# Optimization experiments

Measured on AMD Instinct MI355X. Metric: run time of the kernel, lower is better.

The kernel has to match this reference:

```python
import jax, jax.numpy as jnp
import numpy as np

DIM = 1024
HEADS = 16
HEAD_DIM = DIM // HEADS
SCALE = HEAD_DIM ** -0.5


def setup_inputs() -> dict:
    key = jax.random.key(0)
    ks = jax.random.split(key, 6)
    B, N = 2, 2048
    s = DIM ** -0.5
    return {
        "x": jax.random.normal(ks[0], (B, N, DIM), dtype=jnp.float32),
        "Wq": jax.random.normal(ks[1], (DIM, DIM), dtype=jnp.float32) * s,
        "Wk": jax.random.normal(ks[2], (DIM, DIM), dtype=jnp.float32) * s,
        "Wv": jax.random.normal(ks[3], (DIM, DIM), dtype=jnp.float32) * s,
        "Wo": jax.random.normal(ks[4], (DIM, DIM), dtype=jnp.float32) * s,
        "bo": jnp.zeros((DIM,), dtype=jnp.float32),
    }


def reference(x, Wq, Wk, Wv, Wo, bo):
    B, N, D = x.shape
    # Linear projections (torch Linear: y = x @ W.T)
    q = x @ Wq.T
    k = x @ Wk.T
    v = x @ Wv.T
    # [B, H, N, hd]
    q = q.reshape(B, N, HEADS, HEAD_DIM).transpose(0, 2, 1, 3)
    k = k.reshape(B, N, HEADS, HEAD_DIM).transpose(0, 2, 1, 3)
    v = v.reshape(B, N, HEADS, HEAD_DIM).transpose(0, 2, 1, 3)
    scores = jnp.einsum('bhid,bhjd->bhij', q, k) * SCALE
    probs = jax.nn.softmax(scores, axis=-1)
    out = jnp.einsum('bhij,bhjd->bhid', probs, v)
    out = out.transpose(0, 2, 1, 3).reshape(B, N, D)
    return out @ Wo.T + bo
```

## Files before the change

kernel.cpp:

```cpp
#include <hip/hip_runtime.h>

#define DIM    1024
#define HEADS  16
#define HD     64
#define BATCH  2
#define SEQ    2048
#define C2     0.18033688011112042f

typedef __attribute__((ext_vector_type(8))) short           short8;
typedef __attribute__((ext_vector_type(4))) short           short4v;
typedef __attribute__((ext_vector_type(4))) float           f4;
typedef __attribute__((ext_vector_type(4))) unsigned short  u16x4;
typedef __attribute__((ext_vector_type(4))) unsigned int    u32x4;
typedef __attribute__((ext_vector_type(2))) unsigned int    u32x2;

typedef __attribute__((address_space(3))) unsigned int       as3_u32;
typedef const __attribute__((address_space(1))) unsigned int as1_u32;

__device__ __forceinline__ unsigned short f2bf(float f) {
    unsigned int u = __builtin_bit_cast(unsigned int, f);
    u = (u + 0x7fffu + ((u >> 16) & 1u)) >> 16;
    return (unsigned short)u;
}
__device__ __forceinline__ unsigned int pk_bf16(float a, float b) {
    return (unsigned int)f2bf(a) | ((unsigned int)f2bf(b) << 16);
}
__device__ __forceinline__ unsigned int pk_bf16_hw(float a, float b) {
    unsigned int r;
    asm("v_cvt_pk_bf16_f32 %0, %1, %2" : "=v"(r) : "v"(a), "v"(b));
    return r;
}

#if __has_builtin(__builtin_amdgcn_exp2f)
#define EXP2(x) __builtin_amdgcn_exp2f(x)
#else
#define EXP2(x) exp2f(x)
#endif

__device__ __forceinline__ void gl2lds16(const unsigned short* g, unsigned short* l) {
    __builtin_amdgcn_global_load_lds((as1_u32*)g, (as3_u32*)l, 16, 0, 0);
}

__global__ __launch_bounds__(256) void k_cast_all(
    const float* __restrict__ x,  const float* __restrict__ wq,
    const float* __restrict__ wk, const float* __restrict__ wv,
    const float* __restrict__ wo, unsigned short* __restrict__ dst)
{
    const int i = blockIdx.x * 256 + threadIdx.x;
    const float* src;
    int off;
    if (i < (1 << 20))            { src = x;  off = 0; }
    else if (i < (5 << 18))       { src = wq; off = 1 << 20; }
    else if (i < (6 << 18))       { src = wk; off = 5 << 18; }
    else if (i < (7 << 18))       { src = wv; off = 6 << 18; }
    else                          { src = wo; off = 7 << 18; }
    f4 v = ((const f4*)src)[i - off];
    u16x4 o;
    o[0] = f2bf(v[0]); o[1] = f2bf(v[1]); o[2] = f2bf(v[2]); o[3] = f2bf(v[3]);
    ((u16x4*)dst)[i] = o;
}

__global__ __launch_bounds__(256) void gemm_qkv(
    const unsigned short* __restrict__ A,
    const unsigned short* __restrict__ Wq,
    const unsigned short* __restrict__ Wk,
    const unsigned short* __restrict__ Wv,
    unsigned short* __restrict__ Qo,
    unsigned short* __restrict__ Ko,
    unsigned short* __restrict__ Vo)
{
    __shared__ __align__(16) unsigned short Xs[128 * 32];
    __shared__ __align__(16) unsigned short Ws[128 * 32];
    const int L   = blockIdx.x;
    const int xcd = L & 7;
    const int idx = L >> 3;
    const int col = idx >> 2;
    const int sb  = (xcd * 4 + (idx & 3)) * 128;
    const int wsel = col >> 3;
    const int fb   = (col & 7) * 128;
    const unsigned short* W = (wsel == 0) ? Wq : ((wsel == 1) ? Wk : Wv);

    const int tid  = threadIdx.x;
    const int wave = tid >> 6, lane = tid & 63;
    const int quad = lane >> 4, l16 = lane & 15;
    const int wm = (wave & 1) << 6, wn = (wave >> 1) << 6;

    const unsigned short* aLDS = (wsel < 2) ? Ws : Xs;
    const unsigned short* bLDS = (wsel < 2) ? Xs : Ws;

    f4 acc[4][4] = {};

    for (int k0 = 0; k0 < DIM; k0 += 32) {
        __syncthreads();
        #pragma unroll
        for (int i = 0; i < 2; i++) {
            const int c = tid + (i << 8);
            const int row = c >> 2, koff = (c & 3) << 3;
            gl2lds16(&A[(size_t)(sb + row) * DIM + k0 + koff], &Xs[(size_t)((i << 8) + (wave << 6)) * 8]);
            gl2lds16(&W[(size_t)(fb + row) * DIM + k0 + koff], &Ws[(size_t)((i << 8) + (wave << 6)) * 8]);
        }
        __syncthreads();
        short8 afr[4], bfr[4];
        #pragma unroll
        for (int i = 0; i < 4; i++)
            afr[i] = *(const short8*)(&aLDS[(wm + i * 16 + l16) * 32 + quad * 8]);
        #pragma unroll
        for (int j = 0; j < 4; j++)
            bfr[j] = *(const short8*)(&bLDS[(wn + j * 16 + l16) * 32 + quad * 8]);
        #pragma unroll
        for (int i = 0; i < 4; i++)
            #pragma unroll
            for (int j = 0; j < 4; j++)
                acc[i][j] = __builtin_amdgcn_mfma_f32_16x16x32_bf16(afr[i], bfr[j], acc[i][j], 0, 0, 0);
    }

    if (wsel < 2) {
        unsigned short* out = (wsel == 0) ? Qo : Ko;
        const float sc = (wsel == 0) ? C2 : 1.0f;
        #pragma unroll
        for (int j = 0; j < 4; j++) {
            const int ms = sb + wn + j * 16 + l16;
            const int b = ms >> 11, ns = ms & (SEQ - 1);
            #pragma unroll
            for (int i = 0; i < 4; i++) {
                const int feat = fb + wm + i * 16 + quad * 4;
                const int h = feat >> 6, d = feat & (HD - 1);
                u32x2 pw;
                pw[0] = pk_bf16(acc[i][j][0] * sc, acc[i][j][1] * sc);
                pw[1] = pk_bf16(acc[i][j][2] * sc, acc[i][j][3] * sc);
                *(u32x2*)(&out[((size_t)(b * HEADS + h) * SEQ + ns) * HD + d]) = pw;
            }
        }
    } else {
        #pragma unroll
        for (int j = 0; j < 4; j++) {
            const int feat = fb + wn + j * 16 + l16;
            const int h = feat >> 6, d = feat & (HD - 1);
            #pragma unroll
            for (int i = 0; i < 4; i++) {
                const int ms = sb + wm + i * 16 + quad * 4;
                const int b = ms >> 11, ns = ms & (SEQ - 1);
                u32x2 pw;
                pw[0] = pk_bf16(acc[i][j][0], acc[i][j][1]);
                pw[1] = pk_bf16(acc[i][j][2], acc[i][j][3]);
                *(u32x2*)(&Vo[((size_t)(b * HEADS + h) * HD + d) * SEQ + ns]) = pw;
            }
        }
    }
}

__global__ __launch_bounds__(256, 2) void attn_fwd(
    const unsigned short* __restrict__ Qg,
    const unsigned short* __restrict__ Kg,
    const unsigned short* __restrict__ VTg,
    unsigned short* __restrict__ AOb)
{
    __shared__ __align__(16) unsigned short Ks [2][64 * 72];
    __shared__ __align__(16) unsigned short VsT[2][64 * 72];
#if !__has_builtin(__builtin_amdgcn_mfma_f32_16x16x16bf16_1k)
    __shared__ __align__(16) unsigned short Ps[128 * 72];
#endif

    const int L   = blockIdx.x;
    const int xcd = L & 7;
    const int idx = L >> 3;
    const int bh  = xcd * 4 + (idx >> 4);
    const int q0  = (idx & 15) << 7;

    const unsigned short* Qb  = Qg  + (size_t)bh * SEQ * HD;
    const unsigned short* Kb  = Kg  + (size_t)bh * SEQ * HD;
    const unsigned short* VTb = VTg + (size_t)bh * HD * SEQ;

    const int tid  = threadIdx.x;
    const int wave = tid >> 6, lane = tid & 63;
    const int quad = lane >> 4, l16 = lane & 15;
    const int qw   = wave << 5;
    const int r8   = tid >> 3;
    const int g8   = (tid & 7) * 8;

    short8 qf[2][2];
    #pragma unroll
    for (int nf = 0; nf < 2; nf++)
        #pragma unroll
        for (int ks = 0; ks < 2; ks++)
            qf[nf][ks] = *(const short8*)(&Qb[(size_t)(q0 + qw + nf * 16 + l16) * HD + ks * 32 + quad * 8]);

    #pragma unroll
    for (int p = 0; p < 2; p++) {
        const int row = r8 + p * 32;
        *(u32x4*)(&Ks [0][row * 72 + g8]) = *(const u32x4*)(&Kb [(size_t)row * HD + g8]);
        *(u32x4*)(&VsT[0][row * 72 + g8]) = *(const u32x4*)(&VTb[(size_t)row * SEQ + g8]);
    }
    __syncthreads();

    f4 lsum[2] = {};
    f4 Oacc[4][2] = {};
    int cur = 0;

    for (int kt = 0; kt < SEQ / 64; kt++) {
        u32x4 kpre[2], vpre[2];
        if (kt < SEQ / 64 - 1) {
            #pragma unroll
            for (int p = 0; p < 2; p++) {
                const int row = r8 + p * 32;
                kpre[p] = *(const u32x4*)(&Kb [(size_t)((kt + 1) * 64 + row) * HD + g8]);
                vpre[p] = *(const u32x4*)(&VTb[(size_t)row * SEQ + (kt + 1) * 64 + g8]);
            }
        }
        const unsigned short* ksb = &Ks [cur][0];
        const unsigned short* vsb = &VsT[cur][0];

        f4 sacc[4][2] = {};
        __builtin_amdgcn_s_setprio(1);
        #pragma unroll
        for (int ks = 0; ks < 2; ks++) {
            short8 kfr[4];
            #pragma unroll
            for (int mf = 0; mf < 4; mf++)
                kfr[mf] = *(const short8*)(&ksb[(mf * 16 + l16) * 72 + ks * 32 + quad * 8]);
            #pragma unroll
            for (int mf = 0; mf < 4; mf++)
                #pragma unroll
                for (int nf = 0; nf < 2; nf++)
                    sacc[mf][nf] = __builtin_amdgcn_mfma_f32_16x16x32_bf16(kfr[mf], qf[nf][ks], sacc[mf][nf], 0, 0, 0);
        }
        __builtin_amdgcn_s_setprio(0);

#if __has_builtin(__builtin_amdgcn_mfma_f32_16x16x16bf16_1k)
        #pragma unroll
        for (int mf = 0; mf < 4; mf++) {
            short4v vfr[4];
            #pragma unroll
            for (int d = 0; d < 4; d++)
                vfr[d] = *(const short4v*)(&vsb[(d * 16 + l16) * 72 + mf * 16 + quad * 4]);
            short4v pbx[2];
            #pragma unroll
            for (int nf = 0; nf < 2; nf++) {
                f4 pv;
                #pragma unroll
                for (int r = 0; r < 4; r++)
                    pv[r] = EXP2(sacc[mf][nf][r]);
                lsum[nf] += pv;
                u32x2 pw;
                pw[0] = pk_bf16_hw(pv[0], pv[1]);
                pw[1] = pk_bf16_hw(pv[2], pv[3]);
                pbx[nf] = __builtin_bit_cast(short4v, pw);
            }
            #pragma unroll
            for (int d = 0; d < 4; d++)
                #pragma unroll
                for (int nf = 0; nf < 2; nf++)
                    Oacc[d][nf] = __builtin_amdgcn_mfma_f32_16x16x16bf16_1k(vfr[d], pbx[nf], Oacc[d][nf], 0, 0, 0);
        }
#else
        #pragma unroll
        for (int nf = 0; nf < 2; nf++) {
            #pragma unroll
            for (int mf = 0; mf < 4; mf++) {
                f4 pv;
                #pragma unroll
                for (int r = 0; r < 4; r++)
                    pv[r] = EXP2(sacc[mf][nf][r]);
                lsum[nf] += pv;
                u32x2 pw;
                pw[0] = pk_bf16(pv[0], pv[1]);
                pw[1] = pk_bf16(pv[2], pv[3]);
                *(u32x2*)(&Ps[(qw + nf * 16 + l16) * 72 + mf * 16 + quad * 4]) = pw;
            }
        }
        #pragma unroll
        for (int ks = 0; ks < 2; ks++) {
            short8 vfr[4], pf[2];
            #pragma unroll
            for (int mf = 0; mf < 4; mf++)
                vfr[mf] = *(const short8*)(&vsb[(mf * 16 + l16) * 72 + ks * 32 + quad * 8]);
            #pragma unroll
            for (int nf = 0; nf < 2; nf++)
                pf[nf] = *(const short8*)(&Ps[(qw + nf * 16 + l16) * 72 + ks * 32 + quad * 8]);
            #pragma unroll
            for (int mf = 0; mf < 4; mf++)
                #pragma unroll
                for (int nf = 0; nf < 2; nf++)
                    Oacc[mf][nf] = __builtin_amdgcn_mfma_f32_16x16x32_bf16(vfr[mf], pf[nf], Oacc[mf][nf], 0, 0, 0);
        }
#endif

        if (kt < SEQ / 64 - 1) {
            #pragma unroll
            for (int p = 0; p < 2; p++) {
                const int row = r8 + p * 32;
                *(u32x4*)(&Ks [cur ^ 1][row * 72 + g8]) = kpre[p];
                *(u32x4*)(&VsT[cur ^ 1][row * 72 + g8]) = vpre[p];
            }
            __syncthreads();
        }
        cur ^= 1;
    }

    const int b = bh >> 4, h = bh & (HEADS - 1);
    #pragma unroll
    for (int nf = 0; nf < 2; nf++) {
        float l = lsum[nf][0] + lsum[nf][1] + lsum[nf][2] + lsum[nf][3];
        l += __shfl_xor(l, 16);
        l += __shfl_xor(l, 32);
        const float inv = 1.0f / l;
        const int qg = q0 + qw + nf * 16 + l16;
        #pragma unroll
        for (int mf = 0; mf < 4; mf++) {
            u32x2 o;
            o[0] = pk_bf16_hw(Oacc[mf][nf][0] * inv, Oacc[mf][nf][1] * inv);
            o[1] = pk_bf16_hw(Oacc[mf][nf][2] * inv, Oacc[mf][nf][3] * inv);
            *(u32x2*)(&AOb[(size_t)(b * SEQ + qg) * DIM + h * HD + mf * 16 + quad * 4]) = o;
        }
    }
}

__global__ __launch_bounds__(256) void gemm_out(
    const unsigned short* __restrict__ AO,
    const unsigned short* __restrict__ W,
    float* __restrict__ out,
    const float* __restrict__ bias)
{
    __shared__ __align__(16) unsigned short As[64 * 32];
    __shared__ __align__(16) unsigned short Bs[128 * 32];
    const int L   = blockIdx.x;
    const int xcd = L & 7;
    const int idx = L >> 3;
    const int n0  = (xcd * 4 + (idx >> 4)) * 128;
    const int m0  = (idx & 15) * 64;

    const int tid  = threadIdx.x;
    const int wave = tid >> 6, lane = tid & 63;
    const int quad = lane >> 4, l16 = lane & 15;
    const int wm = (wave & 1) << 5, wn = (wave >> 1) << 6;

    f4 acc[2][4] = {};

    for (int k0 = 0; k0 < DIM; k0 += 32) {
        __syncthreads();
        gl2lds16(&W[(size_t)(m0 + (tid >> 2)) * DIM + k0 + ((tid & 3) << 3)],
                 &As[(size_t)(wave << 6) * 8]);
        #pragma unroll
        for (int i = 0; i < 2; i++) {
            const int c = tid + (i << 8);
            gl2lds16(&AO[(size_t)(n0 + (c >> 2)) * DIM + k0 + ((c & 3) << 3)],
                     &Bs[(size_t)((i << 8) + (wave << 6)) * 8]);
        }
        __syncthreads();
        short8 afr[2], bfr[4];
        #pragma unroll
        for (int i = 0; i < 2; i++)
            afr[i] = *(const short8*)(&As[(wm + i * 16 + l16) * 32 + quad * 8]);
        #pragma unroll
        for (int j = 0; j < 4; j++)
            bfr[j] = *(const short8*)(&Bs[(wn + j * 16 + l16) * 32 + quad * 8]);
        #pragma unroll
        for (int i = 0; i < 2; i++)
            #pragma unroll
            for (int j = 0; j < 4; j++)
                acc[i][j] = __builtin_amdgcn_mfma_f32_16x16x32_bf16(afr[i], bfr[j], acc[i][j], 0, 0, 0);
    }

    #pragma unroll
    for (int i = 0; i < 2; i++) {
        const int feat = m0 + wm + i * 16 + quad * 4;
        const f4 bv = *(const f4*)(&bias[feat]);
        #pragma unroll
        for (int j = 0; j < 4; j++) {
            const int ns = n0 + wn + j * 16 + l16;
            *(f4*)(&out[(size_t)ns * DIM + feat]) = acc[i][j] + bv;
        }
    }
}

extern "C" void kernel_launch(void* const* d_in, const int* in_sizes, int n_in,
                              void* d_out, int out_size, void* d_ws, size_t ws_size,
                              hipStream_t stream) {
    (void)in_sizes; (void)n_in; (void)out_size; (void)ws_size;
    const float* x  = (const float*)d_in[0];
    const float* Wq = (const float*)d_in[1];
    const float* Wk = (const float*)d_in[2];
    const float* Wv = (const float*)d_in[3];
    const float* Wo = (const float*)d_in[4];
    const float* bo = (const float*)d_in[5];

    unsigned short* wsu = (unsigned short*)d_ws;
    unsigned short* xb  = wsu;
    unsigned short* Wqb = wsu + (4u  << 20);
    unsigned short* Wkb = wsu + (5u  << 20);
    unsigned short* Wvb = wsu + (6u  << 20);
    unsigned short* Wob = wsu + (7u  << 20);
    unsigned short* Qb  = wsu + (8u  << 20);
    unsigned short* Kb  = wsu + (12u << 20);
    unsigned short* VTb = wsu + (16u << 20);
    unsigned short* AOb = wsu + (20u << 20);

    k_cast_all<<<8192, 256, 0, stream>>>(x, Wq, Wk, Wv, Wo, wsu);

    gemm_qkv<<<768, 256, 0, stream>>>(xb, Wqb, Wkb, Wvb, Qb, Kb, VTb);

    attn_fwd<<<512, 256, 0, stream>>>(Qb, Kb, VTb, AOb);

    gemm_out<<<512, 256, 0, stream>>>(AOb, Wob, (float*)d_out, bo);
}
```

Measured before the change: 179.7 us.

## Double-buffer LDS tiles in QKV and output projection GEMMs

Both projection GEMMs now keep two LDS tile buffers. The global-to-LDS load for the next k-step is issued before the MFMAs on the current buffer, and the loop drops from two barriers per iteration to one. The aim is to hide global load latency behind matrix math. LDS use per block doubles, which may lower occupancy, and correctness depends on the barrier also waiting for the async LDS-DMA loads to finish.

Result: slower. 183.6 us (+2.2%).

```diff
diff --git a/kernel.cpp b/kernel.cpp
--- a/kernel.cpp
+++ b/kernel.cpp
@@ -69,8 +69,8 @@
     unsigned short* __restrict__ Ko,
     unsigned short* __restrict__ Vo)
 {
-    __shared__ __align__(16) unsigned short Xs[128 * 32];
-    __shared__ __align__(16) unsigned short Ws[128 * 32];
+    __shared__ __align__(16) unsigned short Xs[2][128 * 32];
+    __shared__ __align__(16) unsigned short Ws[2][128 * 32];
     const int L   = blockIdx.x;
     const int xcd = L & 7;
     const int idx = L >> 3;
@@ -85,21 +85,27 @@
     const int quad = lane >> 4, l16 = lane & 15;
     const int wm = (wave & 1) << 6, wn = (wave >> 1) << 6;
 
-    const unsigned short* aLDS = (wsel < 2) ? Ws : Xs;
-    const unsigned short* bLDS = (wsel < 2) ? Xs : Ws;
-
-    f4 acc[4][4] = {};
-
-    for (int k0 = 0; k0 < DIM; k0 += 32) {
-        __syncthreads();
+    auto STAGE = [&](int buf, int k0) {
         #pragma unroll
         for (int i = 0; i < 2; i++) {
             const int c = tid + (i << 8);
             const int row = c >> 2, koff = (c & 3) << 3;
-            gl2lds16(&A[(size_t)(sb + row) * DIM + k0 + koff], &Xs[(size_t)((i << 8) + (wave << 6)) * 8]);
-            gl2lds16(&W[(size_t)(fb + row) * DIM + k0 + koff], &Ws[(size_t)((i << 8) + (wave << 6)) * 8]);
-        }
-        __syncthreads();
+            gl2lds16(&A[(size_t)(sb + row) * DIM + k0 + koff], &Xs[buf][(size_t)((i << 8) + (wave << 6)) * 8]);
+            gl2lds16(&W[(size_t)(fb + row) * DIM + k0 + koff], &Ws[buf][(size_t)((i << 8) + (wave << 6)) * 8]);
+        }
+    };
+
+    f4 acc[4][4] = {};
+    int cur = 0;
+
+    STAGE(0, 0);
+    asm volatile("s_waitcnt vmcnt(0)" ::: "memory");
+    __syncthreads();
+
+    for (int k0 = 0; k0 < DIM; k0 += 32) {
+        if (k0 + 32 < DIM) STAGE(cur ^ 1, k0 + 32);
+        const unsigned short* aLDS = (wsel < 2) ? &Ws[cur][0] : &Xs[cur][0];
+        const unsigned short* bLDS = (wsel < 2) ? &Xs[cur][0] : &Ws[cur][0];
         short8 afr[4], bfr[4];
         #pragma unroll
         for (int i = 0; i < 4; i++)
@@ -112,6 +118,8 @@
             #pragma unroll
             for (int j = 0; j < 4; j++)
                 acc[i][j] = __builtin_amdgcn_mfma_f32_16x16x32_bf16(afr[i], bfr[j], acc[i][j], 0, 0, 0);
+        __syncthreads();
+        cur ^= 1;
     }
 
     if (wsel < 2) {
@@ -321,8 +329,8 @@
     float* __restrict__ out,
     const float* __restrict__ bias)
 {
-    __shared__ __align__(16) unsigned short As[64 * 32];
-    __shared__ __align__(16) unsigned short Bs[128 * 32];
+    __shared__ __align__(16) unsigned short As[2][64 * 32];
+    __shared__ __align__(16) unsigned short Bs[2][128 * 32];
     const int L   = blockIdx.x;
     const int xcd = L & 7;
     const int idx = L >> 3;
@@ -334,31 +342,40 @@
     const int quad = lane >> 4, l16 = lane & 15;
     const int wm = (wave & 1) << 5, wn = (wave >> 1) << 6;
 
-    f4 acc[2][4] = {};
-
-    for (int k0 = 0; k0 < DIM; k0 += 32) {
-        __syncthreads();
+    auto STAGE = [&](int buf, int k0) {
         gl2lds16(&W[(size_t)(m0 + (tid >> 2)) * DIM + k0 + ((tid & 3) << 3)],
-                 &As[(size_t)(wave << 6) * 8]);
+                 &As[buf][(size_t)(wave << 6) * 8]);
         #pragma unroll
         for (int i = 0; i < 2; i++) {
             const int c = tid + (i << 8);
             gl2lds16(&AO[(size_t)(n0 + (c >> 2)) * DIM + k0 + ((c & 3) << 3)],
-                     &Bs[(size_t)((i << 8) + (wave << 6)) * 8]);
-        }
-        __syncthreads();
+                     &Bs[buf][(size_t)((i << 8) + (wave << 6)) * 8]);
+        }
+    };
+
+    f4 acc[2][4] = {};
+    int cur = 0;
+
+    STAGE(0, 0);
+    asm volatile("s_waitcnt vmcnt(0)" ::: "memory");
+    __syncthreads();
+
+    for (int k0 = 0; k0 < DIM; k0 += 32) {
+        if (k0 + 32 < DIM) STAGE(cur ^ 1, k0 + 32);
         short8 afr[2], bfr[4];
         #pragma unroll
         for (int i = 0; i < 2; i++)
-            afr[i] = *(const short8*)(&As[(wm + i * 16 + l16) * 32 + quad * 8]);
+            afr[i] = *(const short8*)(&As[cur][(wm + i * 16 + l16) * 32 + quad * 8]);
         #pragma unroll
         for (int j = 0; j < 4; j++)
-            bfr[j] = *(const short8*)(&Bs[(wn + j * 16 + l16) * 32 + quad * 8]);
+            bfr[j] = *(const short8*)(&Bs[cur][(wn + j * 16 + l16) * 32 + quad * 8]);
         #pragma unroll
         for (int i = 0; i < 2; i++)
             #pragma unroll
             for (int j = 0; j < 4; j++)
                 acc[i][j] = __builtin_amdgcn_mfma_f32_16x16x32_bf16(afr[i], bfr[j], acc[i][j], 0, 0, 0);
+        __syncthreads();
+        cur ^= 1;
     }
 
     #pragma unroll
```

## Split key tiles across wave pairs and double attention grid with LDS reduction

Applied to the files above, without the earlier changes.

The attention kernel now processes 64 queries per block instead of 128. Each pair of waves shares 32 queries and splits every 64-key tile into halves, and the partial output and row-sum accumulators are combined through shared memory at the end. The grid doubles and the launch bounds target 4 blocks per CU to raise occupancy and fill more CUs. In exchange, K/V tiles are loaded from global memory twice as often overall, and an extra LDS reduction and syncs are added at the end.

After: 186.5 us. 3.8% more time.

```diff
diff --git a/kernel.cpp b/kernel.cpp
--- a/kernel.cpp
+++ b/kernel.cpp
@@ -149,7 +149,7 @@
     }
 }
 
-__global__ __launch_bounds__(256, 2) void attn_fwd(
+__global__ __launch_bounds__(256, 4) void attn_fwd(
     const unsigned short* __restrict__ Qg,
     const unsigned short* __restrict__ Kg,
     const unsigned short* __restrict__ VTg,
@@ -158,14 +158,14 @@
     __shared__ __align__(16) unsigned short Ks [2][64 * 72];
     __shared__ __align__(16) unsigned short VsT[2][64 * 72];
 #if !__has_builtin(__builtin_amdgcn_mfma_f32_16x16x16bf16_1k)
-    __shared__ __align__(16) unsigned short Ps[128 * 72];
+    __shared__ __align__(16) unsigned short Ps[64 * 72];
 #endif
 
     const int L   = blockIdx.x;
     const int xcd = L & 7;
     const int idx = L >> 3;
-    const int bh  = xcd * 4 + (idx >> 4);
-    const int q0  = (idx & 15) << 7;
+    const int bh  = xcd * 4 + (idx >> 5);
+    const int q0  = (idx & 31) << 6;
 
     const unsigned short* Qb  = Qg  + (size_t)bh * SEQ * HD;
     const unsigned short* Kb  = Kg  + (size_t)bh * SEQ * HD;
@@ -174,7 +174,9 @@
     const int tid  = threadIdx.x;
     const int wave = tid >> 6, lane = tid & 63;
     const int quad = lane >> 4, l16 = lane & 15;
-    const int qw   = wave << 5;
+    const int qh   = wave >> 1;
+    const int kh   = wave & 1;
+    const int qw   = qh << 5;
     const int r8   = tid >> 3;
     const int g8   = (tid & 7) * 8;
 
@@ -210,36 +212,36 @@
         const unsigned short* ksb = &Ks [cur][0];
         const unsigned short* vsb = &VsT[cur][0];
 
-        f4 sacc[4][2] = {};
+        f4 sacc[2][2] = {};
         __builtin_amdgcn_s_setprio(1);
         #pragma unroll
         for (int ks = 0; ks < 2; ks++) {
-            short8 kfr[4];
-            #pragma unroll
-            for (int mf = 0; mf < 4; mf++)
-                kfr[mf] = *(const short8*)(&ksb[(mf * 16 + l16) * 72 + ks * 32 + quad * 8]);
-            #pragma unroll
-            for (int mf = 0; mf < 4; mf++)
+            short8 kfr[2];
+            #pragma unroll
+            for (int m = 0; m < 2; m++)
+                kfr[m] = *(const short8*)(&ksb[((kh * 2 + m) * 16 + l16) * 72 + ks * 32 + quad * 8]);
+            #pragma unroll
+            for (int m = 0; m < 2; m++)
                 #pragma unroll
                 for (int nf = 0; nf < 2; nf++)
-                    sacc[mf][nf] = __builtin_amdgcn_mfma_f32_16x16x32_bf16(kfr[mf], qf[nf][ks], sacc[mf][nf], 0, 0, 0);
+                    sacc[m][nf] = __builtin_amdgcn_mfma_f32_16x16x32_bf16(kfr[m], qf[nf][ks], sacc[m][nf], 0, 0, 0);
         }
         __builtin_amdgcn_s_setprio(0);
 
 #if __has_builtin(__builtin_amdgcn_mfma_f32_16x16x16bf16_1k)
         #pragma unroll
-        for (int mf = 0; mf < 4; mf++) {
+        for (int s = 0; s < 2; s++) {
             short4v vfr[4];
             #pragma unroll
             for (int d = 0; d < 4; d++)
-                vfr[d] = *(const short4v*)(&vsb[(d * 16 + l16) * 72 + mf * 16 + quad * 4]);
+                vfr[d] = *(const short4v*)(&vsb[(d * 16 + l16) * 72 + (kh * 2 + s) * 16 + quad * 4]);
             short4v pbx[2];
             #pragma unroll
             for (int nf = 0; nf < 2; nf++) {
                 f4 pv;
                 #pragma unroll
                 for (int r = 0; r < 4; r++)
-                    pv[r] = EXP2(sacc[mf][nf][r]);
+                    pv[r] = EXP2(sacc[s][nf][r]);
                 lsum[nf] += pv;
                 u32x2 pw;
                 pw[0] = pk_bf16_hw(pv[0], pv[1]);
@@ -254,34 +256,28 @@
         }
 #else
         #pragma unroll
-        for (int nf = 0; nf < 2; nf++) {
-            #pragma unroll
-            for (int mf = 0; mf < 4; mf++) {
+        for (int s = 0; s < 2; s++) {
+            #pragma unroll
+            for (int nf = 0; nf < 2; nf++) {
                 f4 pv;
                 #pragma unroll
                 for (int r = 0; r < 4; r++)
-                    pv[r] = EXP2(sacc[mf][nf][r]);
+                    pv[r] = EXP2(sacc[s][nf][r]);
                 lsum[nf] += pv;
                 u32x2 pw;
                 pw[0] = pk_bf16(pv[0], pv[1]);
                 pw[1] = pk_bf16(pv[2], pv[3]);
-                *(u32x2*)(&Ps[(qw + nf * 16 + l16) * 72 + mf * 16 + quad * 4]) = pw;
-            }
-        }
-        #pragma unroll
-        for (int ks = 0; ks < 2; ks++) {
-            short8 vfr[4], pf[2];
-            #pragma unroll
-            for (int mf = 0; mf < 4; mf++)
-                vfr[mf] = *(const short8*)(&vsb[(mf * 16 + l16) * 72 + ks * 32 + quad * 8]);
-            #pragma unroll
-            for (int nf = 0; nf < 2; nf++)
-                pf[nf] = *(const short8*)(&Ps[(qw + nf * 16 + l16) * 72 + ks * 32 + quad * 8]);
-            #pragma unroll
-            for (int mf = 0; mf < 4; mf++)
-                #pragma unroll
-                for (int nf = 0; nf < 2; nf++)
-                    Oacc[mf][nf] = __builtin_amdgcn_mfma_f32_16x16x32_bf16(vfr[mf], pf[nf], Oacc[mf][nf], 0, 0, 0);
+                *(u32x2*)(&Ps[(qw + nf * 16 + l16) * 72 + (kh * 2 + s) * 16 + quad * 4]) = pw;
+            }
+        }
+        #pragma unroll
+        for (int d = 0; d < 4; d++) {
+            short8 vfr8 = *(const short8*)(&vsb[(d * 16 + l16) * 72 + kh * 32 + quad * 8]);
+            #pragma unroll
+            for (int nf = 0; nf < 2; nf++) {
+                short8 pf8 = *(const short8*)(&Ps[(qw + nf * 16 + l16) * 72 + kh * 32 + quad * 8]);
+                Oacc[d][nf] = __builtin_amdgcn_mfma_f32_16x16x32_bf16(vfr8, pf8, Oacc[d][nf], 0, 0, 0);
+            }
         }
 #endif
 
@@ -297,20 +293,47 @@
         cur ^= 1;
     }
 
-    const int b = bh >> 4, h = bh & (HEADS - 1);
-    #pragma unroll
-    for (int nf = 0; nf < 2; nf++) {
-        float l = lsum[nf][0] + lsum[nf][1] + lsum[nf][2] + lsum[nf][3];
-        l += __shfl_xor(l, 16);
-        l += __shfl_xor(l, 32);
-        const float inv = 1.0f / l;
-        const int qg = q0 + qw + nf * 16 + l16;
-        #pragma unroll
-        for (int mf = 0; mf < 4; mf++) {
-            u32x2 o;
-            o[0] = pk_bf16_hw(Oacc[mf][nf][0] * inv, Oacc[mf][nf][1] * inv);
-            o[1] = pk_bf16_hw(Oacc[mf][nf][2] * inv, Oacc[mf][nf][3] * inv);
-            *(u32x2*)(&AOb[(size_t)(b * SEQ + qg) * DIM + h * HD + mf * 16 + quad * 4]) = o;
+    __syncthreads();
+    float* dO = (float*)&Ks[0][0];
+    float* dL = (float*)&VsT[0][0];
+    if (kh == 1) {
+        const int ob = (qh * 64 + lane) * 36;
+        #pragma unroll
+        for (int mf = 0; mf < 4; mf++)
+            #pragma unroll
+            for (int nf = 0; nf < 2; nf++)
+                *(f4*)(&dO[ob + (mf * 2 + nf) * 4]) = Oacc[mf][nf];
+        const int lb = (qh * 64 + lane) * 8;
+        *(f4*)(&dL[lb])     = lsum[0];
+        *(f4*)(&dL[lb + 4]) = lsum[1];
+    }
+    __syncthreads();
+    if (kh == 0) {
+        const int ob = (qh * 64 + lane) * 36;
+        #pragma unroll
+        for (int mf = 0; mf < 4; mf++)
+            #pragma unroll
+            for (int nf = 0; nf < 2; nf++)
+                Oacc[mf][nf] += *(const f4*)(&dO[ob + (mf * 2 + nf) * 4]);
+        const int lb = (qh * 64 + lane) * 8;
+        lsum[0] += *(const f4*)(&dL[lb]);
+        lsum[1] += *(const f4*)(&dL[lb + 4]);
+
+        const int b = bh >> 4, h = bh & (HEADS - 1);
+        #pragma unroll
+        for (int nf = 0; nf < 2; nf++) {
+            float l = lsum[nf][0] + lsum[nf][1] + lsum[nf][2] + lsum[nf][3];
+            l += __shfl_xor(l, 16);
+            l += __shfl_xor(l, 32);
+            const float inv = 1.0f / l;
+            const int qg = q0 + qw + nf * 16 + l16;
+            #pragma unroll
+            for (int mf = 0; mf < 4; mf++) {
+                u32x2 o;
+                o[0] = pk_bf16_hw(Oacc[mf][nf][0] * inv, Oacc[mf][nf][1] * inv);
+                o[1] = pk_bf16_hw(Oacc[mf][nf][2] * inv, Oacc[mf][nf][3] * inv);
+                *(u32x2*)(&AOb[(size_t)(b * SEQ + qg) * DIM + h * HD + mf * 16 + quad * 4]) = o;
+            }
         }
     }
 }
@@ -399,7 +422,7 @@
 
     gemm_qkv<<<768, 256, 0, stream>>>(xb, Wqb, Wkb, Wvb, Qb, Kb, VTb);
 
-    attn_fwd<<<512, 256, 0, stream>>>(Qb, Kb, VTb, AOb);
+    attn_fwd<<<1024, 256, 0, stream>>>(Qb, Kb, VTb, AOb);
 
     gemm_out<<<512, 256, 0, stream>>>(AOb, Wob, (float*)d_out, bo);
 }
```
